# Performance work log

Hardware: AMD Instinct MI355X
Metric: run time of the kernel (lower is better)

## Reference

```python
import jax, jax.numpy as jnp
import numpy as np

S = 4          # num_segments
T = 4096       # frames
D = 1024       # input_size == output_size
HEADS = 1
FREQ = 10000.0
DH = D // HEADS     # per-head width = 1024
TB = T // S         # block height = 1024
WB = DH // S        # block width  = 256


def _abs_pos(tb, d, freq):
    # Matches getAbsolutePosition: AP[p, 2i] = sin(p / freq^(2i/d)), AP[p, 2i+1] = cos(same).
    pos = jnp.arange(tb, dtype=jnp.float32)[:, None]          # [tb,1]
    i = jnp.arange(tb // 2, dtype=jnp.float32)[None, :]       # [1,tb//2]
    ang = pos / jnp.power(jnp.float32(freq), 2.0 * i / d)     # [tb,tb//2]
    ap = jnp.zeros((tb, tb), jnp.float32)
    return ap.at[:, 0::2].set(jnp.sin(ang)).at[:, 1::2].set(jnp.cos(ang))


def setup_inputs() -> dict:
    key = jax.random.key(0)
    ks = jax.random.split(key, 6)
    x = jax.random.normal(ks[0], (T, D), jnp.float32)
    Wq = jax.random.normal(ks[1], (HEADS, DH, D), jnp.float32) * 0.02
    Wk = jax.random.normal(ks[2], (HEADS, DH, D), jnp.float32) * 0.02
    Wv = jax.random.normal(ks[3], (HEADS, DH, D), jnp.float32) * 0.02
    Wout = jax.random.normal(ks[4], (D, D), jnp.float32) * 0.02
    Wout2 = jax.random.normal(ks[5], (WB, WB + 2), jnp.float32) * 0.05
    return {"x": x, "Wq": Wq, "Wk": Wk, "Wv": Wv, "Wout": Wout, "Wout2": Wout2}


def _forward(x, Wq, Wk, Wv, Wout, Wout2):
    # diversity = 1 - cosine similarity (F.normalize p=2 along dim=1)
    xu = x / jnp.maximum(jnp.linalg.norm(x, axis=1, keepdims=True), 1e-12)
    div = 1.0 - xu @ xu.T                                     # [T,T]

    Q = jnp.einsum('ti,hdi->htd', x, Wq)                      # [h,T,DH]
    K = jnp.einsum('ti,hdi->htd', x, Wk)
    V = jnp.einsum('ti,hdi->htd', x, Wv)

    def blk(A):  # [h,T,DH] -> [h,S*S,TB,WB], block (i,j) row-major as in local_x/local_y
        return A.reshape(-1, S, TB, S, WB).transpose(0, 1, 3, 2, 4).reshape(-1, S * S, TB, WB)

    qb, kb, vb = blk(Q), blk(K), blk(V)
    # diversity uses the diagonal row-block for every column-block j of row i
    drow = jnp.stack([div[i * TB:(i + 1) * TB, i * TB:(i + 1) * TB] for i in range(S)], 0)  # [S,TB,TB]
    db = jnp.repeat(drow, S, axis=0)[None]                    # [1,S*S,TB,TB]

    sim = jnp.einsum('hbqc,hbkc->hbqk', qb, kb) + _abs_pos(TB, D, FREQ)  # [h,S*S,TB,TB]
    attw = jax.nn.softmax(sim, axis=-1)
    # normalized row entropy, then L1-normalized (F.normalize p=1)
    ent = -(attw * jax.nn.log_softmax(sim, axis=-1)).sum(-1) / jnp.log(jnp.float32(TB))  # [h,S*S,TB]
    ent = ent / jnp.maximum(jnp.abs(ent).sum(-1, keepdims=True), 1e-12)

    dep = (db * attw).sum(-1) / db.sum(-1)                    # [h,S*S,TB]
    att_win = attw + dep[:, :, None, :] * attw                # dep_factor rows are identical
    ctx = jnp.einsum('hbqk,hbkc->hbqc', att_win, vb)          # [h,S*S,TB,WB]

    chars = jax.lax.stop_gradient(jnp.stack([ent, dep], axis=-1))  # [h,S*S,TB,2] (detach)
    y = jnp.concatenate([ctx, chars], axis=-1) @ Wout2.T      # [h,S*S,TB,WB]

    # reassemble grid of blocks back to [h,T,DH], concat heads, final projection
    y = y.reshape(-1, S, S, TB, WB).transpose(0, 1, 3, 2, 4).reshape(-1, T, DH)
    y = y.transpose(1, 0, 2).reshape(T, HEADS * DH)
    return y @ Wout.T                                         # [T,D]


def reference(x, Wq, Wk, Wv, Wout, Wout2):
    return _forward(x, Wq, Wk, Wv, Wout, Wout2)
```

## Files before the change

### kernel.cpp

```cpp
#include <hip/hip_runtime.h>
#include <hip/hip_bf16.h>

#define TT 4096
#define DD 1024
#define TBB 1024
#define WBB 256

typedef __attribute__((ext_vector_type(8))) _Float16 half8;
typedef __attribute__((ext_vector_type(4))) _Float16 half4;
typedef __attribute__((ext_vector_type(16))) float f32x16;

__device__ __forceinline__ unsigned short f2h(float v) {
  _Float16 h = (_Float16)v;
  return *reinterpret_cast<unsigned short*>(&h);
}
__device__ __forceinline__ float h2f(unsigned short u) {
  _Float16 h = *reinterpret_cast<_Float16*>(&u);
  return (float)h;
}

__device__ __forceinline__ void gl_lds16(const unsigned short* g, unsigned short* l) {
  __builtin_amdgcn_global_load_lds(
      (const __attribute__((address_space(1))) void*)(unsigned long long)(g),
      (__attribute__((address_space(3))) void*)(unsigned long long)(l),
      16, 0, 0);
}

__device__ __forceinline__ float waveSum(float v) {
#pragma unroll
  for (int o = 32; o > 0; o >>= 1) v += __shfl_down(v, o, 64);
  return v;
}
__device__ __forceinline__ float waveMax(float v) {
#pragma unroll
  for (int o = 32; o > 0; o >>= 1) v = fmaxf(v, __shfl_down(v, o, 64));
  return v;
}

template <int EPI, typename OutT>
__global__ __launch_bounds__(256) void gemm_bt(
    const unsigned short* __restrict__ A, const unsigned short* __restrict__ B,
    OutT* __restrict__ C,
    int K, int lda, int ldb, int ldc,
    int zbase, int zdiv,
    long sAi, long sAj, long sBi, long sBj, long sCi, long sCj,
    long sAz, long sBz, long sCz,
    const float* __restrict__ e0, const float* __restrict__ e1,
    const float* __restrict__ e2, const float* __restrict__ e3)
{
  __shared__ __align__(16) unsigned short lA[2][4096];
  __shared__ __align__(16) unsigned short lB[2][4096];

  const int z = blockIdx.z, gz = zbase + z;
  const int zi = gz / zdiv, zj = gz - zi * zdiv;
  const unsigned short* Ab = A + (long)zi * sAi + (long)zj * sAj + (long)z * sAz;
  const unsigned short* Bb = B + (long)zi * sBi + (long)zj * sBj + (long)z * sBz;
  const long offC = (long)zi * sCi + (long)zj * sCj + (long)z * sCz;

  const int m0 = blockIdx.y * 128, n0 = blockIdx.x * 128;
  const int tid = threadIdx.x, wave = tid >> 6, lane = tid & 63;
  const int wm = (wave >> 1) * 64, wn = (wave & 1) * 64;
  const int srow = lane >> 2;
  const int scol = (((lane & 3) ^ ((srow >> 1) & 3))) * 8;
  const int l31 = lane & 31, khi = lane >> 5;
  const int sw2 = (l31 >> 1) & 3;

  f32x16 acc[2][2] = {};

  for (int k0 = 0; k0 < K; k0 += 64) {
#pragma unroll
    for (int h = 0; h < 2; ++h)
#pragma unroll
      for (int t = 0; t < 2; ++t) {
        const int r = wave * 32 + t * 16 + srow;
        gl_lds16(Ab + (long)(m0 + r) * lda + (k0 + h * 32 + scol), &lA[h][wave * 1024 + t * 512]);
        gl_lds16(Bb + (long)(n0 + r) * ldb + (k0 + h * 32 + scol), &lB[h][wave * 1024 + t * 512]);
      }
    __syncthreads();

    half8 af[2][4], bfr[2][4];
#pragma unroll
    for (int mi = 0; mi < 2; ++mi)
#pragma unroll
      for (int ks = 0; ks < 4; ++ks)
        af[mi][ks] = *(const half8*)&lA[ks >> 1][(wm + mi * 32 + l31) * 32 + ((((ks & 1) * 2 + khi) ^ sw2) * 8)];
#pragma unroll
    for (int ni = 0; ni < 2; ++ni)
#pragma unroll
      for (int ks = 0; ks < 4; ++ks)
        bfr[ni][ks] = *(const half8*)&lB[ks >> 1][(wn + ni * 32 + l31) * 32 + ((((ks & 1) * 2 + khi) ^ sw2) * 8)];

#pragma unroll
    for (int ks = 0; ks < 4; ++ks)
#pragma unroll
      for (int mi = 0; mi < 2; ++mi)
#pragma unroll
        for (int ni = 0; ni < 2; ++ni)
          acc[mi][ni] = __builtin_amdgcn_mfma_f32_32x32x16_f16(af[mi][ks], bfr[ni][ks], acc[mi][ni], 0, 0, 0);
    __syncthreads();
  }

  OutT* Cb = C + offC;
#pragma unroll
  for (int mi = 0; mi < 2; ++mi)
#pragma unroll
    for (int ni = 0; ni < 2; ++ni)
#pragma unroll
      for (int r = 0; r < 16; ++r) {
        const int row = m0 + wm + mi * 32 + khi * 4 + (r & 3) + 8 * (r >> 2);
        const int col = n0 + wn + ni * 32 + l31;
        float v = acc[mi][ni][r];
        const long ci = (long)row * ldc + col;
        if constexpr (sizeof(OutT) == 2) {
          Cb[ci] = (OutT)f2h(v);
        } else {
          Cb[ci] = v;
        }
      }
}

template <int EPI, typename OutT>
__global__ __launch_bounds__(256) void gemm_s(
    const unsigned short* __restrict__ A, const unsigned short* __restrict__ B,
    OutT* __restrict__ C,
    int K, int lda, int ldb, int ldc,
    int zbase, int zdiv,
    long sAi, long sAj, long sBi, long sBj, long sCi, long sCj,
    long sAz, long sBz, long sCz,
    const float* __restrict__ e0, const float* __restrict__ e1,
    const float* __restrict__ e2, const float* __restrict__ e3)
{
  __shared__ __align__(16) unsigned short lA[2][2048];
  __shared__ __align__(16) unsigned short lB[2][2048];

  const int z = blockIdx.z, gz = zbase + z;
  const int zi = gz / zdiv, zj = gz - zi * zdiv;
  const unsigned short* Ab = A + (long)zi * sAi + (long)zj * sAj + (long)z * sAz;
  const unsigned short* Bb = B + (long)zi * sBi + (long)zj * sBj + (long)z * sBz;
  const long offC = (long)zi * sCi + (long)zj * sCj + (long)z * sCz;

  const int m0 = blockIdx.y * 64, n0 = blockIdx.x * 64;
  const int tid = threadIdx.x, wave = tid >> 6, lane = tid & 63;
  const int wm = (wave >> 1) * 32, wn = (wave & 1) * 32;
  const int srow = lane >> 2;
  const int grow = wave * 16 + srow;
  const int scol = (((lane & 3) ^ ((grow >> 1) & 3))) * 8;
  const int l31 = lane & 31, khi = lane >> 5;
  const int sw2 = (l31 >> 1) & 3;

  f32x16 acc = {};

  for (int k0 = 0; k0 < K; k0 += 64) {
#pragma unroll
    for (int h = 0; h < 2; ++h) {
      gl_lds16(Ab + (long)(m0 + grow) * lda + (k0 + h * 32 + scol), &lA[h][wave * 512]);
      gl_lds16(Bb + (long)(n0 + grow) * ldb + (k0 + h * 32 + scol), &lB[h][wave * 512]);
    }
    __syncthreads();

    half8 af[4], bfr[4];
#pragma unroll
    for (int ks = 0; ks < 4; ++ks) {
      af[ks] = *(const half8*)&lA[ks >> 1][(wm + l31) * 32 + ((((ks & 1) * 2 + khi) ^ sw2) * 8)];
      bfr[ks] = *(const half8*)&lB[ks >> 1][(wn + l31) * 32 + ((((ks & 1) * 2 + khi) ^ sw2) * 8)];
    }
#pragma unroll
    for (int ks = 0; ks < 4; ++ks)
      acc = __builtin_amdgcn_mfma_f32_32x32x16_f16(af[ks], bfr[ks], acc, 0, 0, 0);
    __syncthreads();
  }

  OutT* Cb = C + offC;
#pragma unroll
  for (int r = 0; r < 16; ++r) {
    const int row = m0 + wm + khi * 4 + (r & 3) + 8 * (r >> 2);
    const int col = n0 + wn + l31;
    float v = acc[r];
    if constexpr (EPI == 1) v = 1.0f - v;
    if constexpr (EPI == 3)
      v += e0[(long)gz * 1024 + row] * e2[col] + e1[(long)gz * 1024 + row] * e3[col];
    const long ci = (long)row * ldc + col;
    if constexpr (sizeof(OutT) == 2) {
      Cb[ci] = (OutT)f2h(v);
    } else {
      Cb[ci] = v;
    }
  }
}

__global__ __launch_bounds__(256) void sim_gemm(
    const unsigned short* __restrict__ A, const unsigned short* __restrict__ B,
    unsigned short* __restrict__ C,
    const unsigned short* __restrict__ APh)
{
  __shared__ __align__(16) unsigned short lA[2][4096];
  __shared__ __align__(16) unsigned short lB[2][4096];

  const int gz = blockIdx.z;
  const int zi = gz >> 2, zj = gz & 3;
  const unsigned short* Ab = A + (long)zi * (TBB * DD) + zj * WBB;
  const unsigned short* Bb = B + (long)zi * (TBB * DD) + zj * WBB;
  unsigned short* Cb = C + (long)gz * TBB * TBB;

  const int m0 = blockIdx.y * 128, n0 = blockIdx.x * 128;
  const int tid = threadIdx.x, wave = tid >> 6, lane = tid & 63;
  const int wm = (wave >> 1) * 64, wn = (wave & 1) * 64;
  const int srow = lane >> 2;
  const int scol = ((lane & 3) ^ ((srow >> 1) & 3)) * 8;
  const int l31 = lane & 31, khi = lane >> 5;
  const int sw2 = (l31 >> 1) & 3;

  f32x16 acc[2][2] = {};

  for (int k0 = 0; k0 < WBB; k0 += 64) {
#pragma unroll
    for (int h = 0; h < 2; ++h)
#pragma unroll
      for (int t = 0; t < 2; ++t) {
        const int r = wave * 32 + t * 16 + srow;
        gl_lds16(Ab + (long)(m0 + r) * DD + (k0 + h * 32 + scol), &lA[h][wave * 1024 + t * 512]);
        gl_lds16(Bb + (long)(n0 + r) * DD + (k0 + h * 32 + scol), &lB[h][wave * 1024 + t * 512]);
      }
    __syncthreads();

    half8 af[2][4], bfr[2][4];
#pragma unroll
    for (int mi = 0; mi < 2; ++mi)
#pragma unroll
      for (int ks = 0; ks < 4; ++ks)
        af[mi][ks] = *(const half8*)&lA[ks >> 1][(wm + mi * 32 + l31) * 32 + ((((ks & 1) * 2 + khi) ^ sw2) * 8)];
#pragma unroll
    for (int ni = 0; ni < 2; ++ni)
#pragma unroll
      for (int ks = 0; ks < 4; ++ks)
        bfr[ni][ks] = *(const half8*)&lB[ks >> 1][(wn + ni * 32 + l31) * 32 + ((((ks & 1) * 2 + khi) ^ sw2) * 8)];

#pragma unroll
    for (int ks = 0; ks < 4; ++ks)
#pragma unroll
      for (int mi = 0; mi < 2; ++mi)
#pragma unroll
        for (int ni = 0; ni < 2; ++ni)
          acc[mi][ni] = __builtin_amdgcn_mfma_f32_32x32x16_f16(af[mi][ks], bfr[ni][ks], acc[mi][ni], 0, 0, 0);
    __syncthreads();
  }

#pragma unroll
  for (int mi = 0; mi < 2; ++mi)
#pragma unroll
    for (int ni = 0; ni < 2; ++ni)
#pragma unroll
      for (int r = 0; r < 16; ++r) {
        const int row = m0 + wm + mi * 32 + khi * 4 + (r & 3) + 8 * (r >> 2);
        const int col = n0 + wn + ni * 32 + l31;
        Cb[(long)row * TBB + col] = f2h(acc[mi][ni][r] + h2f(APh[(long)row * 1024 + col]));
      }
}

__global__ __launch_bounds__(256) void ctx_gemm_s(
    const unsigned short* __restrict__ wpre, const float* __restrict__ dep,
    const unsigned short* __restrict__ Vt, unsigned short* __restrict__ ctx)
{
  __shared__ __align__(16) unsigned short lA[2][2048];
  __shared__ __align__(16) unsigned short lB[2][2048];
  __shared__ __align__(16) unsigned short sDepH[1024];

  const int gz = blockIdx.z, zi = gz >> 2, zj = gz & 3;
  const int m0 = blockIdx.y * 64, n0 = blockIdx.x * 64;
  const int tid = threadIdx.x, wave = tid >> 6, lane = tid & 63;
  const int wm = (wave >> 1) * 32, wn = (wave & 1) * 32;
  const int srow = lane >> 2;
  const int grow = wave * 16 + srow;
  const int scol = ((lane & 3) ^ ((grow >> 1) & 3)) * 8;
  const int l31 = lane & 31, khi = lane >> 5;
  const int sw2 = (l31 >> 1) & 3;

#pragma unroll
  for (int p = 0; p < 4; ++p)
    sDepH[tid + p * 256] = f2h(1.f + dep[(long)gz * 1024 + tid + p * 256]);
  __syncthreads();

  const unsigned short* Ab = wpre + (long)gz * TBB * TBB;
  const unsigned short* Bb = Vt + (long)(zj * 256) * TT + (long)zi * 1024;

  f32x16 acc = {};

  for (int k0 = 0; k0 < 1024; k0 += 64) {
#pragma unroll
    for (int h = 0; h < 2; ++h)
      gl_lds16(Bb + (long)(n0 + grow) * TT + (k0 + h * 32 + scol), &lB[h][wave * 512]);
#pragma unroll
    for (int h = 0; h < 2; ++h)
#pragma unroll
      for (int p = 0; p < 2; ++p) {
        const int idx = p * 1024 + tid * 4;
        const int row = idx >> 5, col = idx & 31;
        ushort4 wv = *(const ushort4*)(Ab + (long)(m0 + row) * 1024 + k0 + h * 32 + col);
        const half4 dv = *(const half4*)&sDepH[k0 + h * 32 + col];
        half4 pv = *(half4*)&wv * dv;
        const int pcol = (((col >> 3) ^ ((row >> 1) & 3)) << 3) | (col & 7);
        *(half4*)&lA[h][row * 32 + pcol] = pv;
      }
    __syncthreads();

    half8 af[4], bfr[4];
#pragma unroll
    for (int ks = 0; ks < 4; ++ks) {
      af[ks] = *(const half8*)&lA[ks >> 1][(wm + l31) * 32 + ((((ks & 1) * 2 + khi) ^ sw2) * 8)];
      bfr[ks] = *(const half8*)&lB[ks >> 1][(wn + l31) * 32 + ((((ks & 1) * 2 + khi) ^ sw2) * 8)];
    }
#pragma unroll
    for (int ks = 0; ks < 4; ++ks)
      acc = __builtin_amdgcn_mfma_f32_32x32x16_f16(af[ks], bfr[ks], acc, 0, 0, 0);
    __syncthreads();
  }

  unsigned short* Cb = ctx + (long)gz * TBB * WBB;
#pragma unroll
  for (int r = 0; r < 16; ++r) {
    const int row = m0 + wm + khi * 4 + (r & 3) + 8 * (r >> 2);
    const int col = n0 + wn + l31;
    Cb[(long)row * WBB + col] = f2h(acc[r]);
  }
}

__global__ __launch_bounds__(256) void prepx_kernel(
    const float* __restrict__ x, unsigned short* __restrict__ xh,
    unsigned short* __restrict__ xu)
{
  const int t = blockIdx.x, tid = threadIdx.x;
  const float4 v = *((const float4*)(x + (long)t * DD) + tid);
  float ss = v.x * v.x + v.y * v.y + v.z * v.z + v.w * v.w;
  ss = waveSum(ss);
  __shared__ float red[4];
  if ((tid & 63) == 0) red[tid >> 6] = ss;
  __syncthreads();
  const float tot = red[0] + red[1] + red[2] + red[3];
  const float inv = 1.f / fmaxf(sqrtf(tot), 1e-12f);
  ushort4 h, u;
  h.x = f2h(v.x); h.y = f2h(v.y); h.z = f2h(v.z); h.w = f2h(v.w);
  u.x = f2h(v.x * inv); u.y = f2h(v.y * inv); u.z = f2h(v.z * inv); u.w = f2h(v.w * inv);
  *((ushort4*)(xh + (long)t * DD) + tid) = h;
  *((ushort4*)(xu + (long)t * DD) + tid) = u;
}

__global__ __launch_bounds__(256) void castw_kernel(
    const float* __restrict__ Wq, const float* __restrict__ Wk, const float* __restrict__ Wv,
    unsigned short* __restrict__ o)
{
  const long idx4 = ((long)blockIdx.x * 256 + threadIdx.x) * 4;
  const int which = (int)(idx4 >> 20);
  const long loc = idx4 & ((1L << 20) - 1);
  const float* src = (which == 0) ? Wq : ((which == 1) ? Wk : Wv);
  const float4 v = *(const float4*)(src + loc);
  ushort4 h;
  h.x = f2h(v.x); h.y = f2h(v.y); h.z = f2h(v.z); h.w = f2h(v.w);
  *(ushort4*)(o + idx4) = h;
}

__global__ __launch_bounds__(256) void castp_kernel(const float* __restrict__ src,
                                                    unsigned short* __restrict__ dst)
{
  const long idx4 = ((long)blockIdx.x * 256 + threadIdx.x) * 4;
  const float4 v = *(const float4*)(src + idx4);
  ushort4 h;
  h.x = f2h(v.x); h.y = f2h(v.y); h.z = f2h(v.z); h.w = f2h(v.w);
  *(ushort4*)(dst + idx4) = h;
}

__global__ __launch_bounds__(256) void packw2_kernel(
    const float* __restrict__ W2, unsigned short* __restrict__ W2B,
    float* __restrict__ Ecol, float* __restrict__ Dcol)
{
  const int c = blockIdx.x, j = threadIdx.x;
  W2B[c * 256 + j] = f2h(W2[c * 258 + j]);
  if (j == 0) {
    Ecol[c] = W2[c * 258 + 256];
    Dcol[c] = W2[c * 258 + 257];
  }
}

__global__ __launch_bounds__(256) void ap_kernel(unsigned short* __restrict__ APh)
{
  const int p = blockIdx.x, tid = threadIdx.x;
#pragma unroll
  for (int t = 0; t < 4; ++t) {
    const int col = tid + t * 256;
    const int i = col >> 1;
    const float e = (2.0f * (float)i) / 1024.0f;
    const float ang = (float)p / powf(10000.0f, e);
    APh[(long)p * 1024 + col] = f2h((col & 1) ? cosf(ang) : sinf(ang));
  }
}

__global__ __launch_bounds__(256) void transpose_kernel(
    const unsigned short* __restrict__ V, unsigned short* __restrict__ Vt)
{
  __shared__ unsigned short tile[32][33];
  const int tx = threadIdx.x & 31, ty = threadIdx.x >> 5;
  const int c0 = blockIdx.x * 32;
  const int r0 = blockIdx.y * 32;
#pragma unroll
  for (int rr = ty; rr < 32; rr += 8)
    tile[rr][tx] = V[(long)(r0 + rr) * DD + c0 + tx];
  __syncthreads();
#pragma unroll
  for (int rr = ty; rr < 32; rr += 8)
    Vt[(long)(c0 + rr) * TT + r0 + tx] = tile[tx][rr];
}

__global__ __launch_bounds__(256) void stats_kernel(
    const unsigned short* __restrict__ sim, const unsigned short* __restrict__ divb,
    float* __restrict__ dep, float* __restrict__ ent,
    unsigned short* __restrict__ wpre)
{
  const int q = blockIdx.x, gz = blockIdx.y, bi = gz >> 2;
  const int tid = threadIdx.x;
  const unsigned short* srow = sim + ((long)gz * TBB + q) * TBB;
  const unsigned short* drow = divb + ((long)bi * TBB + q) * TBB;
  const ushort4 sv = ((const ushort4*)srow)[tid];
  const ushort4 dv = ((const ushort4*)drow)[tid];
  float s[4] = {h2f(sv.x), h2f(sv.y), h2f(sv.z), h2f(sv.w)};
  float d[4] = {h2f(dv.x), h2f(dv.y), h2f(dv.z), h2f(dv.w)};
  float m = fmaxf(fmaxf(s[0], s[1]), fmaxf(s[2], s[3]));
  m = waveMax(m);
  __shared__ float red[4];
  if ((tid & 63) == 0) red[tid >> 6] = m;
  __syncthreads();
  m = fmaxf(fmaxf(red[0], red[1]), fmaxf(red[2], red[3]));
  float e[4];
  float l = 0.f, ss = 0.f, dn = 0.f, ds = 0.f;
#pragma unroll
  for (int p = 0; p < 4; ++p) {
    e[p] = expf(s[p] - m);
    l += e[p]; ss += e[p] * s[p]; dn += e[p] * d[p]; ds += d[p];
  }
  l = waveSum(l); ss = waveSum(ss); dn = waveSum(dn); ds = waveSum(ds);
  __shared__ float r2[16];
  if ((tid & 63) == 0) {
    const int w = tid >> 6;
    r2[w] = l; r2[4 + w] = ss; r2[8 + w] = dn; r2[12 + w] = ds;
  }
  __syncthreads();
  const float L = r2[0] + r2[1] + r2[2] + r2[3];
  const float Li = 1.f / L;
  ushort4 wq;
  wq.x = f2h(e[0] * Li); wq.y = f2h(e[1] * Li);
  wq.z = f2h(e[2] * Li); wq.w = f2h(e[3] * Li);
  ((ushort4*)(wpre + ((long)gz * TBB + q) * TBB))[tid] = wq;
  if (tid == 0) {
    const float SS = r2[4] + r2[5] + r2[6] + r2[7];
    const float DN = r2[8] + r2[9] + r2[10] + r2[11];
    const float DS = r2[12] + r2[13] + r2[14] + r2[15];
    const long o = (long)gz * TBB + q;
    dep[o] = (DN * Li) / DS;
    ent[o] = (m + logf(L) - SS * Li) * 0.14426950408889634f;
  }
}

__global__ __launch_bounds__(256) void entnorm_kernel(float* __restrict__ ent)
{
  const int gz = blockIdx.x, tid = threadIdx.x;
  float s = 0.f;
#pragma unroll
  for (int p = 0; p < 4; ++p) s += fabsf(ent[(long)gz * TBB + tid + p * 256]);
  s = waveSum(s);
  __shared__ float red[4];
  if ((tid & 63) == 0) red[tid >> 6] = s;
  __syncthreads();
  const float scale = 1.f / fmaxf(red[0] + red[1] + red[2] + red[3], 1e-12f);
#pragma unroll
  for (int p = 0; p < 4; ++p) ent[(long)gz * TBB + tid + p * 256] *= scale;
}

extern "C" void kernel_launch(void* const* d_in, const int* in_sizes, int n_in,
                              void* d_out, int out_size, void* d_ws, size_t ws_size,
                              hipStream_t stream)
{
  const float* x  = (const float*)d_in[0];
  const float* Wq = (const float*)d_in[1];
  const float* Wk = (const float*)d_in[2];
  const float* Wv = (const float*)d_in[3];
  const float* Wo = (const float*)d_in[4];
  const float* W2 = (const float*)d_in[5];

  char* ws = (char*)d_ws;
  size_t off = 0;
  auto take = [&](size_t bytes) -> void* {
    void* p = ws + off;
    off += (bytes + 255) & ~(size_t)255;
    return p;
  };
  unsigned short* QKV = (unsigned short*)take((size_t)3 * TT * DD * 2);
  unsigned short* xh  = (unsigned short*)take((size_t)TT * DD * 2);
  unsigned short* xu  = (unsigned short*)take((size_t)TT * DD * 2);
  unsigned short* Wh  = (unsigned short*)take((size_t)3 * DD * DD * 2);
  unsigned short* WoB = (unsigned short*)take((size_t)DD * DD * 2);
  unsigned short* W2B = (unsigned short*)take((size_t)256 * 256 * 2);
  float* Ecol = (float*)take(256 * 4);
  float* Dcol = (float*)take(256 * 4);
  unsigned short* APh = (unsigned short*)take((size_t)TBB * TBB * 2);
  unsigned short* divb = (unsigned short*)take((size_t)4 * TBB * TBB * 2);
  unsigned short* Vt = (unsigned short*)take((size_t)DD * TT * 2);
  unsigned short* simh = (unsigned short*)take((size_t)16 * TBB * TBB * 2);
  unsigned short* wpre = (unsigned short*)take((size_t)16 * TBB * TBB * 2);
  float* depb = (float*)take((size_t)16 * TBB * 4);
  float* entb = (float*)take((size_t)16 * TBB * 4);
  unsigned short* ctx = (unsigned short*)take((size_t)16 * TBB * WBB * 2);
  unsigned short* Y = (unsigned short*)take((size_t)TT * DD * 2);
  (void)ws_size; (void)in_sizes; (void)n_in; (void)out_size;

  prepx_kernel<<<TT, 256, 0, stream>>>(x, xh, xu);
  castw_kernel<<<(3 * DD * DD) / 1024, 256, 0, stream>>>(Wq, Wk, Wv, Wh);
  castp_kernel<<<(DD * DD) / 1024, 256, 0, stream>>>(Wo, WoB);
  packw2_kernel<<<256, 256, 0, stream>>>(W2, W2B, Ecol, Dcol);
  ap_kernel<<<TBB, 256, 0, stream>>>(APh);

  gemm_bt<0, unsigned short><<<dim3(DD / 128, TT / 128, 3), 256, 0, stream>>>(
      xh, Wh, QKV,
      DD, DD, DD, DD, 0, 1,
      0, 0, (long)DD * DD, 0, (long)TT * DD, 0,
      0, 0, 0, nullptr, nullptr, nullptr, nullptr);

  transpose_kernel<<<dim3(DD / 32, TT / 32), 256, 0, stream>>>(QKV + (size_t)2 * TT * DD, Vt);

  gemm_s<1, unsigned short><<<dim3(16, 16, 4), 256, 0, stream>>>(
      xu, xu, divb,
      DD, DD, DD, TBB, 0, 1,
      (long)TBB * DD, 0, (long)TBB * DD, 0, (long)TBB * TBB, 0,
      0, 0, 0, nullptr, nullptr, nullptr, nullptr);

  const unsigned short* Qh = QKV;
  const unsigned short* Kh = QKV + (size_t)TT * DD;

  sim_gemm<<<dim3(8, 8, 16), 256, 0, stream>>>(Qh, Kh, simh, APh);

  stats_kernel<<<dim3(TBB, 16), 256, 0, stream>>>(simh, divb, depb, entb, wpre);
  entnorm_kernel<<<16, 256, 0, stream>>>(entb);

  ctx_gemm_s<<<dim3(4, 16, 16), 256, 0, stream>>>(wpre, depb, Vt, ctx);

  gemm_s<3, unsigned short><<<dim3(4, 16, 16), 256, 0, stream>>>(
      ctx, W2B, Y,
      WBB, WBB, WBB, DD, 0, 4,
      (long)4 * TBB * WBB, (long)TBB * WBB, 0, 0, (long)TBB * DD, (long)WBB,
      0, 0, 0, entb, depb, Ecol, Dcol);

  gemm_s<0, float><<<dim3(16, 64, 1), 256, 0, stream>>>(
      Y, WoB, (float*)d_out,
      DD, DD, DD, DD, 0, 1,
      0, 0, 0, 0, 0, 0,
      0, 0, 0, nullptr, nullptr, nullptr, nullptr);
}
```

Measured before the change: 266.3 us.

## Fuse softmax statistics into sim GEMM epilogue and recompute exp in ctx GEMM

The sim GEMM epilogue now computes exp(sim) and accumulates per-row sums of exp, exp*sim and exp*div with atomics, and the div GEMM accumulates row sums of div the same way. This replaces the row-wise stats kernel and the separate wpre buffer. The ctx GEMM recomputes the softmax weights from simh, using the 1/L factor and the dependency factor, while it loads the A tile. This removes a full pass over the 16x1024x1024 sim tensor and the write of wpre. In exchange it skips max-subtraction, which risks overflow if logits are large, and adds atomic contention. The Wo cast is also merged into castw, and a small zero kernel is added for the accumulators.

Result: slower. 295.5 us (+11.0%).

```diff
diff --git a/kernel.cpp b/kernel.cpp
--- a/kernel.cpp
+++ b/kernel.cpp
@@ -31,31 +31,20 @@
   for (int o = 32; o > 0; o >>= 1) v += __shfl_down(v, o, 64);
   return v;
 }
-__device__ __forceinline__ float waveMax(float v) {
-#pragma unroll
-  for (int o = 32; o > 0; o >>= 1) v = fmaxf(v, __shfl_down(v, o, 64));
-  return v;
-}
-
-template <int EPI, typename OutT>
+
 __global__ __launch_bounds__(256) void gemm_bt(
     const unsigned short* __restrict__ A, const unsigned short* __restrict__ B,
-    OutT* __restrict__ C,
+    unsigned short* __restrict__ C,
     int K, int lda, int ldb, int ldc,
-    int zbase, int zdiv,
-    long sAi, long sAj, long sBi, long sBj, long sCi, long sCj,
-    long sAz, long sBz, long sCz,
-    const float* __restrict__ e0, const float* __restrict__ e1,
-    const float* __restrict__ e2, const float* __restrict__ e3)
+    long sBz, long sCz)
 {
   __shared__ __align__(16) unsigned short lA[2][4096];
   __shared__ __align__(16) unsigned short lB[2][4096];
 
-  const int z = blockIdx.z, gz = zbase + z;
-  const int zi = gz / zdiv, zj = gz - zi * zdiv;
-  const unsigned short* Ab = A + (long)zi * sAi + (long)zj * sAj + (long)z * sAz;
-  const unsigned short* Bb = B + (long)zi * sBi + (long)zj * sBj + (long)z * sBz;
-  const long offC = (long)zi * sCi + (long)zj * sCj + (long)z * sCz;
+  const int z = blockIdx.z;
+  const unsigned short* Ab = A;
+  const unsigned short* Bb = B + (long)z * sBz;
+  unsigned short* Cb = C + (long)z * sCz;
 
   const int m0 = blockIdx.y * 128, n0 = blockIdx.x * 128;
   const int tid = threadIdx.x, wave = tid >> 6, lane = tid & 63;
@@ -100,7 +89,6 @@
     __syncthreads();
   }
 
-  OutT* Cb = C + offC;
 #pragma unroll
   for (int mi = 0; mi < 2; ++mi)
 #pragma unroll
@@ -109,13 +97,7 @@
       for (int r = 0; r < 16; ++r) {
         const int row = m0 + wm + mi * 32 + khi * 4 + (r & 3) + 8 * (r >> 2);
         const int col = n0 + wn + ni * 32 + l31;
-        float v = acc[mi][ni][r];
-        const long ci = (long)row * ldc + col;
-        if constexpr (sizeof(OutT) == 2) {
-          Cb[ci] = (OutT)f2h(v);
-        } else {
-          Cb[ci] = v;
-        }
+        Cb[(long)row * ldc + col] = f2h(acc[mi][ni][r]);
       }
 }
 
@@ -124,20 +106,20 @@
     const unsigned short* __restrict__ A, const unsigned short* __restrict__ B,
     OutT* __restrict__ C,
     int K, int lda, int ldb, int ldc,
-    int zbase, int zdiv,
+    int zdiv,
     long sAi, long sAj, long sBi, long sBj, long sCi, long sCj,
-    long sAz, long sBz, long sCz,
     const float* __restrict__ e0, const float* __restrict__ e1,
-    const float* __restrict__ e2, const float* __restrict__ e3)
+    const float* __restrict__ e2, const float* __restrict__ e3,
+    float* __restrict__ dsb)
 {
   __shared__ __align__(16) unsigned short lA[2][2048];
   __shared__ __align__(16) unsigned short lB[2][2048];
 
-  const int z = blockIdx.z, gz = zbase + z;
+  const int gz = blockIdx.z;
   const int zi = gz / zdiv, zj = gz - zi * zdiv;
-  const unsigned short* Ab = A + (long)zi * sAi + (long)zj * sAj + (long)z * sAz;
-  const unsigned short* Bb = B + (long)zi * sBi + (long)zj * sBj + (long)z * sBz;
-  const long offC = (long)zi * sCi + (long)zj * sCj + (long)z * sCz;
+  const unsigned short* Ab = A + (long)zi * sAi + (long)zj * sAj;
+  const unsigned short* Bb = B + (long)zi * sBi + (long)zj * sBj;
+  const long offC = (long)zi * sCi + (long)zj * sCj;
 
   const int m0 = blockIdx.y * 64, n0 = blockIdx.x * 64;
   const int tid = threadIdx.x, wave = tid >> 6, lane = tid & 63;
@@ -185,13 +167,20 @@
     } else {
       Cb[ci] = v;
     }
+    if constexpr (EPI == 1) {
+      float pv = v;
+#pragma unroll
+      for (int o = 16; o > 0; o >>= 1) pv += __shfl_down(pv, o, 32);
+      if (l31 == 0) atomicAdd(&dsb[(long)gz * 1024 + row], pv);
+    }
   }
 }
 
 __global__ __launch_bounds__(256) void sim_gemm(
     const unsigned short* __restrict__ A, const unsigned short* __restrict__ B,
-    unsigned short* __restrict__ C,
-    const unsigned short* __restrict__ APh)
+    unsigned short* __restrict__ C, const unsigned short* __restrict__ APh,
+    const unsigned short* __restrict__ divb,
+    float* __restrict__ accL, float* __restrict__ accS, float* __restrict__ accD)
 {
   __shared__ __align__(16) unsigned short lA[2][4096];
   __shared__ __align__(16) unsigned short lB[2][4096];
@@ -201,6 +190,7 @@
   const unsigned short* Ab = A + (long)zi * (TBB * DD) + zj * WBB;
   const unsigned short* Bb = B + (long)zi * (TBB * DD) + zj * WBB;
   unsigned short* Cb = C + (long)gz * TBB * TBB;
+  const unsigned short* Db = divb + (long)(gz >> 2) * TBB * TBB;
 
   const int m0 = blockIdx.y * 128, n0 = blockIdx.x * 128;
   const int tid = threadIdx.x, wave = tid >> 6, lane = tid & 63;
@@ -245,25 +235,48 @@
     __syncthreads();
   }
 
+  float* aL = accL + (long)gz * 1024;
+  float* aS = accS + (long)gz * 1024;
+  float* aD = accD + (long)gz * 1024;
 #pragma unroll
   for (int mi = 0; mi < 2; ++mi)
 #pragma unroll
-    for (int ni = 0; ni < 2; ++ni)
-#pragma unroll
-      for (int r = 0; r < 16; ++r) {
-        const int row = m0 + wm + mi * 32 + khi * 4 + (r & 3) + 8 * (r >> 2);
+    for (int r = 0; r < 16; ++r) {
+      const int row = m0 + wm + mi * 32 + khi * 4 + (r & 3) + 8 * (r >> 2);
+      float pl = 0.f, ps = 0.f, pd = 0.f;
+#pragma unroll
+      for (int ni = 0; ni < 2; ++ni) {
         const int col = n0 + wn + ni * 32 + l31;
-        Cb[(long)row * TBB + col] = f2h(acc[mi][ni][r] + h2f(APh[(long)row * 1024 + col]));
-      }
+        const float v = acc[mi][ni][r] + h2f(APh[(long)row * 1024 + col]);
+        Cb[(long)row * TBB + col] = f2h(v);
+        const float e = expf(v);
+        pl += e;
+        ps += e * v;
+        pd += e * h2f(Db[(long)row * TBB + col]);
+      }
+#pragma unroll
+      for (int o = 16; o > 0; o >>= 1) {
+        pl += __shfl_down(pl, o, 32);
+        ps += __shfl_down(ps, o, 32);
+        pd += __shfl_down(pd, o, 32);
+      }
+      if (l31 == 0) {
+        atomicAdd(&aL[row], pl);
+        atomicAdd(&aS[row], ps);
+        atomicAdd(&aD[row], pd);
+      }
+    }
 }
 
 __global__ __launch_bounds__(256) void ctx_gemm_s(
-    const unsigned short* __restrict__ wpre, const float* __restrict__ dep,
+    const unsigned short* __restrict__ simh, const float* __restrict__ LiB,
+    const float* __restrict__ dep,
     const unsigned short* __restrict__ Vt, unsigned short* __restrict__ ctx)
 {
   __shared__ __align__(16) unsigned short lA[2][2048];
   __shared__ __align__(16) unsigned short lB[2][2048];
-  __shared__ __align__(16) unsigned short sDepH[1024];
+  __shared__ float sLi[64];
+  __shared__ float sDep[1024];
 
   const int gz = blockIdx.z, zi = gz >> 2, zj = gz & 3;
   const int m0 = blockIdx.y * 64, n0 = blockIdx.x * 64;
@@ -275,12 +288,13 @@
   const int l31 = lane & 31, khi = lane >> 5;
   const int sw2 = (l31 >> 1) & 3;
 
+  if (tid < 64) sLi[tid] = LiB[(long)gz * 1024 + m0 + tid];
 #pragma unroll
   for (int p = 0; p < 4; ++p)
-    sDepH[tid + p * 256] = f2h(1.f + dep[(long)gz * 1024 + tid + p * 256]);
+    sDep[tid + p * 256] = 1.f + dep[(long)gz * 1024 + tid + p * 256];
   __syncthreads();
 
-  const unsigned short* Ab = wpre + (long)gz * TBB * TBB;
+  const unsigned short* Ab = simh + (long)gz * TBB * TBB;
   const unsigned short* Bb = Vt + (long)(zj * 256) * TT + (long)zi * 1024;
 
   f32x16 acc = {};
@@ -295,11 +309,15 @@
       for (int p = 0; p < 2; ++p) {
         const int idx = p * 1024 + tid * 4;
         const int row = idx >> 5, col = idx & 31;
-        ushort4 wv = *(const ushort4*)(Ab + (long)(m0 + row) * 1024 + k0 + h * 32 + col);
-        const half4 dv = *(const half4*)&sDepH[k0 + h * 32 + col];
-        half4 pv = *(half4*)&wv * dv;
+        const ushort4 sv = *(const ushort4*)(Ab + (long)(m0 + row) * 1024 + k0 + h * 32 + col);
+        const float li = sLi[row];
+        ushort4 pv;
+        pv.x = f2h(expf(h2f(sv.x)) * li * sDep[k0 + h * 32 + col]);
+        pv.y = f2h(expf(h2f(sv.y)) * li * sDep[k0 + h * 32 + col + 1]);
+        pv.z = f2h(expf(h2f(sv.z)) * li * sDep[k0 + h * 32 + col + 2]);
+        pv.w = f2h(expf(h2f(sv.w)) * li * sDep[k0 + h * 32 + col + 3]);
         const int pcol = (((col >> 3) ^ ((row >> 1) & 3)) << 3) | (col & 7);
-        *(half4*)&lA[h][row * 32 + pcol] = pv;
+        *(ushort4*)&lA[h][row * 32 + pcol] = pv;
       }
     __syncthreads();
 
@@ -322,6 +340,12 @@
     const int col = n0 + wn + l31;
     Cb[(long)row * WBB + col] = f2h(acc[r]);
   }
+}
+
+__global__ __launch_bounds__(256) void zero_kernel(float* __restrict__ p, int n)
+{
+  const int i = blockIdx.x * 256 + threadIdx.x;
+  if (i < n) p[i] = 0.f;
 }
 
 __global__ __launch_bounds__(256) void prepx_kernel(
@@ -346,26 +370,16 @@
 
 __global__ __launch_bounds__(256) void castw_kernel(
     const float* __restrict__ Wq, const float* __restrict__ Wk, const float* __restrict__ Wv,
-    unsigned short* __restrict__ o)
+    const float* __restrict__ Wo, unsigned short* __restrict__ o)
 {
   const long idx4 = ((long)blockIdx.x * 256 + threadIdx.x) * 4;
   const int which = (int)(idx4 >> 20);
   const long loc = idx4 & ((1L << 20) - 1);
-  const float* src = (which == 0) ? Wq : ((which == 1) ? Wk : Wv);
+  const float* src = (which == 0) ? Wq : ((which == 1) ? Wk : ((which == 2) ? Wv : Wo));
   const float4 v = *(const float4*)(src + loc);
   ushort4 h;
   h.x = f2h(v.x); h.y = f2h(v.y); h.z = f2h(v.z); h.w = f2h(v.w);
   *(ushort4*)(o + idx4) = h;
-}
-
-__global__ __launch_bounds__(256) void castp_kernel(const float* __restrict__ src,
-                                                    unsigned short* __restrict__ dst)
-{
-  const long idx4 = ((long)blockIdx.x * 256 + threadIdx.x) * 4;
-  const float4 v = *(const float4*)(src + idx4);
-  ushort4 h;
-  h.x = f2h(v.x); h.y = f2h(v.y); h.z = f2h(v.z); h.w = f2h(v.w);
-  *(ushort4*)(dst + idx4) = h;
 }
 
 __global__ __launch_bounds__(256) void packw2_kernel(
@@ -409,68 +423,33 @@
     Vt[(long)(c0 + rr) * TT + r0 + tx] = tile[tx][rr];
 }
 
-__global__ __launch_bounds__(256) void stats_kernel(
-    const unsigned short* __restrict__ sim, const unsigned short* __restrict__ divb,
-    float* __restrict__ dep, float* __restrict__ ent,
-    unsigned short* __restrict__ wpre)
-{
-  const int q = blockIdx.x, gz = blockIdx.y, bi = gz >> 2;
-  const int tid = threadIdx.x;
-  const unsigned short* srow = sim + ((long)gz * TBB + q) * TBB;
-  const unsigned short* drow = divb + ((long)bi * TBB + q) * TBB;
-  const ushort4 sv = ((const ushort4*)srow)[tid];
-  const ushort4 dv = ((const ushort4*)drow)[tid];
-  float s[4] = {h2f(sv.x), h2f(sv.y), h2f(sv.z), h2f(sv.w)};
-  float d[4] = {h2f(dv.x), h2f(dv.y), h2f(dv.z), h2f(dv.w)};
-  float m = fmaxf(fmaxf(s[0], s[1]), fmaxf(s[2], s[3]));
-  m = waveMax(m);
-  __shared__ float red[4];
-  if ((tid & 63) == 0) red[tid >> 6] = m;
-  __syncthreads();
-  m = fmaxf(fmaxf(red[0], red[1]), fmaxf(red[2], red[3]));
-  float e[4];
-  float l = 0.f, ss = 0.f, dn = 0.f, ds = 0.f;
+__global__ __launch_bounds__(256) void statfin_kernel(
+    const float* __restrict__ accL, const float* __restrict__ accS,
+    const float* __restrict__ accD, const float* __restrict__ dsb,
+    float* __restrict__ LiB, float* __restrict__ dep, float* __restrict__ ent)
+{
+  const int gz = blockIdx.x, tid = threadIdx.x;
+  float er[4];
+  float s = 0.f;
 #pragma unroll
   for (int p = 0; p < 4; ++p) {
-    e[p] = expf(s[p] - m);
-    l += e[p]; ss += e[p] * s[p]; dn += e[p] * d[p]; ds += d[p];
-  }
-  l = waveSum(l); ss = waveSum(ss); dn = waveSum(dn); ds = waveSum(ds);
-  __shared__ float r2[16];
-  if ((tid & 63) == 0) {
-    const int w = tid >> 6;
-    r2[w] = l; r2[4 + w] = ss; r2[8 + w] = dn; r2[12 + w] = ds;
-  }
-  __syncthreads();
-  const float L = r2[0] + r2[1] + r2[2] + r2[3];
-  const float Li = 1.f / L;
-  ushort4 wq;
-  wq.x = f2h(e[0] * Li); wq.y = f2h(e[1] * Li);
-  wq.z = f2h(e[2] * Li); wq.w = f2h(e[3] * Li);
-  ((ushort4*)(wpre + ((long)gz * TBB + q) * TBB))[tid] = wq;
-  if (tid == 0) {
-    const float SS = r2[4] + r2[5] + r2[6] + r2[7];
-    const float DN = r2[8] + r2[9] + r2[10] + r2[11];
-    const float DS = r2[12] + r2[13] + r2[14] + r2[15];
-    const long o = (long)gz * TBB + q;
-    dep[o] = (DN * Li) / DS;
-    ent[o] = (m + logf(L) - SS * Li) * 0.14426950408889634f;
-  }
-}
-
-__global__ __launch_bounds__(256) void entnorm_kernel(float* __restrict__ ent)
-{
-  const int gz = blockIdx.x, tid = threadIdx.x;
-  float s = 0.f;
-#pragma unroll
-  for (int p = 0; p < 4; ++p) s += fabsf(ent[(long)gz * TBB + tid + p * 256]);
+    const int r = tid + p * 256;
+    const long o = (long)gz * 1024 + r;
+    const float L = accL[o];
+    const float Li = 1.f / L;
+    dep[o] = (accD[o] * Li) / dsb[(long)(gz >> 2) * 1024 + r];
+    LiB[o] = Li;
+    er[p] = (logf(L) - accS[o] * Li) * 0.14426950408889634f;
+    s += fabsf(er[p]);
+  }
   s = waveSum(s);
   __shared__ float red[4];
   if ((tid & 63) == 0) red[tid >> 6] = s;
   __syncthreads();
   const float scale = 1.f / fmaxf(red[0] + red[1] + red[2] + red[3], 1e-12f);
 #pragma unroll
-  for (int p = 0; p < 4; ++p) ent[(long)gz * TBB + tid + p * 256] *= scale;
+  for (int p = 0; p < 4; ++p)
+    ent[(long)gz * 1024 + tid + p * 256] = er[p] * scale;
 }
 
 extern "C" void kernel_launch(void* const* d_in, const int* in_sizes, int n_in,
@@ -494,8 +473,8 @@
   unsigned short* QKV = (unsigned short*)take((size_t)3 * TT * DD * 2);
   unsigned short* xh  = (unsigned short*)take((size_t)TT * DD * 2);
   unsigned short* xu  = (unsigned short*)take((size_t)TT * DD * 2);
-  unsigned short* Wh  = (unsigned short*)take((size_t)3 * DD * DD * 2);
-  unsigned short* WoB = (unsigned short*)take((size_t)DD * DD * 2);
+  unsigned short* Wh  = (unsigned short*)take((size_t)4 * DD * DD * 2);
+  unsigned short* WoB = Wh + (size_t)3 * DD * DD;
   unsigned short* W2B = (unsigned short*)take((size_t)256 * 256 * 2);
   float* Ecol = (float*)take(256 * 4);
   float* Dcol = (float*)take(256 * 4);
@@ -503,52 +482,53 @@
   unsigned short* divb = (unsigned short*)take((size_t)4 * TBB * TBB * 2);
   unsigned short* Vt = (unsigned short*)take((size_t)DD * TT * 2);
   unsigned short* simh = (unsigned short*)take((size_t)16 * TBB * TBB * 2);
-  unsigned short* wpre = (unsigned short*)take((size_t)16 * TBB * TBB * 2);
+  float* accL = (float*)take((size_t)16 * TBB * 4);
+  float* accS = (float*)take((size_t)16 * TBB * 4);
+  float* accD = (float*)take((size_t)16 * TBB * 4);
+  float* dsb  = (float*)take((size_t)4 * TBB * 4);
+  float* LiB  = (float*)take((size_t)16 * TBB * 4);
   float* depb = (float*)take((size_t)16 * TBB * 4);
   float* entb = (float*)take((size_t)16 * TBB * 4);
   unsigned short* ctx = (unsigned short*)take((size_t)16 * TBB * WBB * 2);
   unsigned short* Y = (unsigned short*)take((size_t)TT * DD * 2);
   (void)ws_size; (void)in_sizes; (void)n_in; (void)out_size;
 
+  const int nZero = (3 * 16 + 4) * TBB;
+  zero_kernel<<<(nZero + 255) / 256, 256, 0, stream>>>(accL, nZero);
   prepx_kernel<<<TT, 256, 0, stream>>>(x, xh, xu);
-  castw_kernel<<<(3 * DD * DD) / 1024, 256, 0, stream>>>(Wq, Wk, Wv, Wh);
-  castp_kernel<<<(DD * DD) / 1024, 256, 0, stream>>>(Wo, WoB);
+  castw_kernel<<<(4 * DD * DD) / 1024, 256, 0, stream>>>(Wq, Wk, Wv, Wo, Wh);
   packw2_kernel<<<256, 256, 0, stream>>>(W2, W2B, Ecol, Dcol);
   ap_kernel<<<TBB, 256, 0, stream>>>(APh);
 
-  gemm_bt<0, unsigned short><<<dim3(DD / 128, TT / 128, 3), 256, 0, stream>>>(
-      xh, Wh, QKV,
-      DD, DD, DD, DD, 0, 1,
-      0, 0, (long)DD * DD, 0, (long)TT * DD, 0,
-      0, 0, 0, nullptr, nullptr, nullptr, nullptr);
+  gemm_bt<<<dim3(DD / 128, TT / 128, 3), 256, 0, stream>>>(
+      xh, Wh, QKV, DD, DD, DD, DD, (long)DD * DD, (long)TT * DD);
 
   transpose_kernel<<<dim3(DD / 32, TT / 32), 256, 0, stream>>>(QKV + (size_t)2 * TT * DD, Vt);
 
   gemm_s<1, unsigned short><<<dim3(16, 16, 4), 256, 0, stream>>>(
       xu, xu, divb,
-      DD, DD, DD, TBB, 0, 1,
+      DD, DD, DD, TBB, 1,
       (long)TBB * DD, 0, (long)TBB * DD, 0, (long)TBB * TBB, 0,
-      0, 0, 0, nullptr, nullptr, nullptr, nullptr);
+      nullptr, nullptr, nullptr, nullptr, dsb);
 
   const unsigned short* Qh = QKV;
   const unsigned short* Kh = QKV + (size_t)TT * DD;
 
-  sim_gemm<<<dim3(8, 8, 16), 256, 0, stream>>>(Qh, Kh, simh, APh);
-
-  stats_kernel<<<dim3(TBB, 16), 256, 0, stream>>>(simh, divb, depb, entb, wpre);
-  entnorm_kernel<<<16, 256, 0, stream>>>(entb);
-
-  ctx_gemm_s<<<dim3(4, 16, 16), 256, 0, stream>>>(wpre, depb, Vt, ctx);
+  sim_gemm<<<dim3(8, 8, 16), 256, 0, stream>>>(Qh, Kh, simh, APh, divb, accL, accS, accD);
+
+  statfin_kernel<<<16, 256, 0, stream>>>(accL, accS, accD, dsb, LiB, depb, entb);
+
+  ctx_gemm_s<<<dim3(4, 16, 16), 256, 0, stream>>>(simh, LiB, depb, Vt, ctx);
 
   gemm_s<3, unsigned short><<<dim3(4, 16, 16), 256, 0, stream>>>(
       ctx, W2B, Y,
-      WBB, WBB, WBB, DD, 0, 4,
+      WBB, WBB, WBB, DD, 4,
       (long)4 * TBB * WBB, (long)TBB * WBB, 0, 0, (long)TBB * DD, (long)WBB,
-      0, 0, 0, entb, depb, Ecol, Dcol);
+      entb, depb, Ecol, Dcol, nullptr);
 
   gemm_s<0, float><<<dim3(16, 64, 1), 256, 0, stream>>>(
       Y, WoB, (float*)d_out,
-      DD, DD, DD, DD, 0, 1,
+      DD, DD, DD, DD, 1,
       0, 0, 0, 0, 0, 0,
-      0, 0, 0, nullptr, nullptr, nullptr, nullptr);
-}
+      nullptr, nullptr, nullptr, nullptr, nullptr);
+}
```

## Fold Wout2 projection into Wout via precomputed fused weight matrix

Applied to the files above, without the earlier changes.

Precomputes a fused weight Bmat combining Wout with the per-block Wout2 (and its entropy/dependency columns) so the block projection and final projection become one GEMM with K padded to 1088. The ctx GEMM writes directly into the padded activation matrix and a small kernel fills the ent/dep columns. This removes one full GEMM launch and the intermediate Y buffer at the cost of slightly longer K, extra small prep kernels, and fp16 rounding of fused weights.

Measured after the change: 268.6 us. No clear change (+0.9%).

```diff
diff --git a/kernel.cpp b/kernel.cpp
--- a/kernel.cpp
+++ b/kernel.cpp
@@ -5,6 +5,7 @@
 #define DD 1024
 #define TBB 1024
 #define WBB 256
+#define KP 1088
 
 typedef __attribute__((ext_vector_type(8))) _Float16 half8;
 typedef __attribute__((ext_vector_type(4))) _Float16 half4;
@@ -37,25 +38,19 @@
   return v;
 }
 
-template <int EPI, typename OutT>
 __global__ __launch_bounds__(256) void gemm_bt(
     const unsigned short* __restrict__ A, const unsigned short* __restrict__ B,
-    OutT* __restrict__ C,
+    unsigned short* __restrict__ C,
     int K, int lda, int ldb, int ldc,
-    int zbase, int zdiv,
-    long sAi, long sAj, long sBi, long sBj, long sCi, long sCj,
-    long sAz, long sBz, long sCz,
-    const float* __restrict__ e0, const float* __restrict__ e1,
-    const float* __restrict__ e2, const float* __restrict__ e3)
+    long sBz, long sCz)
 {
   __shared__ __align__(16) unsigned short lA[2][4096];
   __shared__ __align__(16) unsigned short lB[2][4096];
 
-  const int z = blockIdx.z, gz = zbase + z;
-  const int zi = gz / zdiv, zj = gz - zi * zdiv;
-  const unsigned short* Ab = A + (long)zi * sAi + (long)zj * sAj + (long)z * sAz;
-  const unsigned short* Bb = B + (long)zi * sBi + (long)zj * sBj + (long)z * sBz;
-  const long offC = (long)zi * sCi + (long)zj * sCj + (long)z * sCz;
+  const int z = blockIdx.z;
+  const unsigned short* Ab = A;
+  const unsigned short* Bb = B + (long)z * sBz;
+  unsigned short* Cb = C + (long)z * sCz;
 
   const int m0 = blockIdx.y * 128, n0 = blockIdx.x * 128;
   const int tid = threadIdx.x, wave = tid >> 6, lane = tid & 63;
@@ -100,7 +95,6 @@
     __syncthreads();
   }
 
-  OutT* Cb = C + offC;
 #pragma unroll
   for (int mi = 0; mi < 2; ++mi)
 #pragma unroll
@@ -109,13 +103,7 @@
       for (int r = 0; r < 16; ++r) {
         const int row = m0 + wm + mi * 32 + khi * 4 + (r & 3) + 8 * (r >> 2);
         const int col = n0 + wn + ni * 32 + l31;
-        float v = acc[mi][ni][r];
-        const long ci = (long)row * ldc + col;
-        if constexpr (sizeof(OutT) == 2) {
-          Cb[ci] = (OutT)f2h(v);
-        } else {
-          Cb[ci] = v;
-        }
+        Cb[(long)row * ldc + col] = f2h(acc[mi][ni][r]);
       }
 }
 
@@ -124,20 +112,17 @@
     const unsigned short* __restrict__ A, const unsigned short* __restrict__ B,
     OutT* __restrict__ C,
     int K, int lda, int ldb, int ldc,
-    int zbase, int zdiv,
-    long sAi, long sAj, long sBi, long sBj, long sCi, long sCj,
-    long sAz, long sBz, long sCz,
-    const float* __restrict__ e0, const float* __restrict__ e1,
-    const float* __restrict__ e2, const float* __restrict__ e3)
+    int zdiv,
+    long sAi, long sAj, long sBi, long sBj, long sCi, long sCj)
 {
   __shared__ __align__(16) unsigned short lA[2][2048];
   __shared__ __align__(16) unsigned short lB[2][2048];
 
-  const int z = blockIdx.z, gz = zbase + z;
+  const int gz = blockIdx.z;
   const int zi = gz / zdiv, zj = gz - zi * zdiv;
-  const unsigned short* Ab = A + (long)zi * sAi + (long)zj * sAj + (long)z * sAz;
-  const unsigned short* Bb = B + (long)zi * sBi + (long)zj * sBj + (long)z * sBz;
-  const long offC = (long)zi * sCi + (long)zj * sCj + (long)z * sCz;
+  const unsigned short* Ab = A + (long)zi * sAi + (long)zj * sAj;
+  const unsigned short* Bb = B + (long)zi * sBi + (long)zj * sBj;
+  const long offC = (long)zi * sCi + (long)zj * sCj;
 
   const int m0 = blockIdx.y * 64, n0 = blockIdx.x * 64;
   const int tid = threadIdx.x, wave = tid >> 6, lane = tid & 63;
@@ -177,8 +162,6 @@
     const int col = n0 + wn + l31;
     float v = acc[r];
     if constexpr (EPI == 1) v = 1.0f - v;
-    if constexpr (EPI == 3)
-      v += e0[(long)gz * 1024 + row] * e2[col] + e1[(long)gz * 1024 + row] * e3[col];
     const long ci = (long)row * ldc + col;
     if constexpr (sizeof(OutT) == 2) {
       Cb[ci] = (OutT)f2h(v);
@@ -259,7 +242,7 @@
 
 __global__ __launch_bounds__(256) void ctx_gemm_s(
     const unsigned short* __restrict__ wpre, const float* __restrict__ dep,
-    const unsigned short* __restrict__ Vt, unsigned short* __restrict__ ctx)
+    const unsigned short* __restrict__ Vt, unsigned short* __restrict__ ctxA)
 {
   __shared__ __align__(16) unsigned short lA[2][2048];
   __shared__ __align__(16) unsigned short lB[2][2048];
@@ -315,12 +298,12 @@
     __syncthreads();
   }
 
-  unsigned short* Cb = ctx + (long)gz * TBB * WBB;
+  unsigned short* Cb = ctxA + (long)zi * 1024 * KP + zj * 256;
 #pragma unroll
   for (int r = 0; r < 16; ++r) {
     const int row = m0 + wm + khi * 4 + (r & 3) + 8 * (r >> 2);
     const int col = n0 + wn + l31;
-    Cb[(long)row * WBB + col] = f2h(acc[r]);
+    Cb[(long)row * KP + col] = f2h(acc[r]);
   }
 }
 
@@ -346,38 +329,67 @@
 
 __global__ __launch_bounds__(256) void castw_kernel(
     const float* __restrict__ Wq, const float* __restrict__ Wk, const float* __restrict__ Wv,
-    unsigned short* __restrict__ o)
+    const float* __restrict__ Wo, unsigned short* __restrict__ o)
 {
   const long idx4 = ((long)blockIdx.x * 256 + threadIdx.x) * 4;
   const int which = (int)(idx4 >> 20);
   const long loc = idx4 & ((1L << 20) - 1);
-  const float* src = (which == 0) ? Wq : ((which == 1) ? Wk : Wv);
+  const float* src = (which == 0) ? Wq : ((which == 1) ? Wk : ((which == 2) ? Wv : Wo));
   const float4 v = *(const float4*)(src + loc);
   ushort4 h;
   h.x = f2h(v.x); h.y = f2h(v.y); h.z = f2h(v.z); h.w = f2h(v.w);
   *(ushort4*)(o + idx4) = h;
 }
 
-__global__ __launch_bounds__(256) void castp_kernel(const float* __restrict__ src,
-                                                    unsigned short* __restrict__ dst)
-{
-  const long idx4 = ((long)blockIdx.x * 256 + threadIdx.x) * 4;
-  const float4 v = *(const float4*)(src + idx4);
-  ushort4 h;
-  h.x = f2h(v.x); h.y = f2h(v.y); h.z = f2h(v.z); h.w = f2h(v.w);
-  *(ushort4*)(dst + idx4) = h;
-}
-
 __global__ __launch_bounds__(256) void packw2_kernel(
-    const float* __restrict__ W2, unsigned short* __restrict__ W2B,
-    float* __restrict__ Ecol, float* __restrict__ Dcol)
-{
-  const int c = blockIdx.x, j = threadIdx.x;
-  W2B[c * 256 + j] = f2h(W2[c * 258 + j]);
-  if (j == 0) {
-    Ecol[c] = W2[c * 258 + 256];
-    Dcol[c] = W2[c * 258 + 257];
-  }
+    const float* __restrict__ W2, unsigned short* __restrict__ W2T)
+{
+  const int c = blockIdx.x, n = threadIdx.x;
+  W2T[c * 256 + n] = f2h(W2[n * 258 + c]);
+}
+
+__global__ __launch_bounds__(256) void bvec_kernel(
+    const float* __restrict__ W2, const unsigned short* __restrict__ WoB,
+    unsigned short* __restrict__ Bmat)
+{
+  const int d = blockIdx.x, tid = threadIdx.x;
+  const int wave = tid >> 6;
+  const float e = W2[tid * 258 + 256], dd = W2[tid * 258 + 257];
+  float p[8];
+#pragma unroll
+  for (int zj = 0; zj < 4; ++zj) {
+    const float w = h2f(WoB[(long)d * 1024 + zj * 256 + tid]);
+    p[zj] = w * e;
+    p[4 + zj] = w * dd;
+  }
+  __shared__ float red[4][8];
+#pragma unroll
+  for (int i = 0; i < 8; ++i) {
+    const float s = waveSum(p[i]);
+    if ((tid & 63) == 0) red[wave][i] = s;
+  }
+  __syncthreads();
+  if (tid < 8) {
+    const float s = red[0][tid] + red[1][tid] + red[2][tid] + red[3][tid];
+    Bmat[(long)d * KP + 1024 + tid] = f2h(s);
+  }
+  if (tid >= 8 && tid < 64) Bmat[(long)d * KP + 1024 + tid] = 0;
+}
+
+__global__ __launch_bounds__(256) void apad_kernel(
+    const float* __restrict__ ent, const float* __restrict__ dep,
+    unsigned short* __restrict__ ctxA)
+{
+  const int t = blockIdx.x * 256 + threadIdx.x;
+  const int zi = t >> 10, row = t & 1023;
+  unsigned short* base = ctxA + (long)t * KP + 1024;
+#pragma unroll
+  for (int zj = 0; zj < 4; ++zj) {
+    base[zj] = f2h(ent[(long)((zi << 2) + zj) * 1024 + row]);
+    base[4 + zj] = f2h(dep[(long)((zi << 2) + zj) * 1024 + row]);
+  }
+#pragma unroll
+  for (int i = 8; i < 64; ++i) base[i] = 0;
 }
 
 __global__ __launch_bounds__(256) void ap_kernel(unsigned short* __restrict__ APh)
@@ -494,11 +506,10 @@
   unsigned short* QKV = (unsigned short*)take((size_t)3 * TT * DD * 2);
   unsigned short* xh  = (unsigned short*)take((size_t)TT * DD * 2);
   unsigned short* xu  = (unsigned short*)take((size_t)TT * DD * 2);
-  unsigned short* Wh  = (unsigned short*)take((size_t)3 * DD * DD * 2);
-  unsigned short* WoB = (unsigned short*)take((size_t)DD * DD * 2);
-  unsigned short* W2B = (unsigned short*)take((size_t)256 * 256 * 2);
-  float* Ecol = (float*)take(256 * 4);
-  float* Dcol = (float*)take(256 * 4);
+  unsigned short* Wh  = (unsigned short*)take((size_t)4 * DD * DD * 2);
+  unsigned short* WoB = Wh + (size_t)3 * DD * DD;
+  unsigned short* W2T = (unsigned short*)take((size_t)256 * 256 * 2);
+  unsigned short* Bmat = (unsigned short*)take((size_t)DD * KP * 2);
   unsigned short* APh = (unsigned short*)take((size_t)TBB * TBB * 2);
   unsigned short* divb = (unsigned short*)take((size_t)4 * TBB * TBB * 2);
   unsigned short* Vt = (unsigned short*)take((size_t)DD * TT * 2);
@@ -506,29 +517,29 @@
   unsigned short* wpre = (unsigned short*)take((size_t)16 * TBB * TBB * 2);
   float* depb = (float*)take((size_t)16 * TBB * 4);
   float* entb = (float*)take((size_t)16 * TBB * 4);
-  unsigned short* ctx = (unsigned short*)take((size_t)16 * TBB * WBB * 2);
-  unsigned short* Y = (unsigned short*)take((size_t)TT * DD * 2);
+  unsigned short* ctxA = (unsigned short*)take((size_t)TT * KP * 2);
   (void)ws_size; (void)in_sizes; (void)n_in; (void)out_size;
 
   prepx_kernel<<<TT, 256, 0, stream>>>(x, xh, xu);
-  castw_kernel<<<(3 * DD * DD) / 1024, 256, 0, stream>>>(Wq, Wk, Wv, Wh);
-  castp_kernel<<<(DD * DD) / 1024, 256, 0, stream>>>(Wo, WoB);
-  packw2_kernel<<<256, 256, 0, stream>>>(W2, W2B, Ecol, Dcol);
+  castw_kernel<<<(4 * DD * DD) / 1024, 256, 0, stream>>>(Wq, Wk, Wv, Wo, Wh);
+  packw2_kernel<<<256, 256, 0, stream>>>(W2, W2T);
   ap_kernel<<<TBB, 256, 0, stream>>>(APh);
 
-  gemm_bt<0, unsigned short><<<dim3(DD / 128, TT / 128, 3), 256, 0, stream>>>(
-      xh, Wh, QKV,
-      DD, DD, DD, DD, 0, 1,
-      0, 0, (long)DD * DD, 0, (long)TT * DD, 0,
-      0, 0, 0, nullptr, nullptr, nullptr, nullptr);
+  gemm_s<0, unsigned short><<<dim3(4, 16, 4), 256, 0, stream>>>(
+      WoB, W2T, Bmat,
+      256, DD, 256, KP, 1,
+      256, 0, 0, 0, 256, 0);
+  bvec_kernel<<<DD, 256, 0, stream>>>(W2, WoB, Bmat);
+
+  gemm_bt<<<dim3(DD / 128, TT / 128, 3), 256, 0, stream>>>(
+      xh, Wh, QKV, DD, DD, DD, DD, (long)DD * DD, (long)TT * DD);
 
   transpose_kernel<<<dim3(DD / 32, TT / 32), 256, 0, stream>>>(QKV + (size_t)2 * TT * DD, Vt);
 
   gemm_s<1, unsigned short><<<dim3(16, 16, 4), 256, 0, stream>>>(
       xu, xu, divb,
-      DD, DD, DD, TBB, 0, 1,
-      (long)TBB * DD, 0, (long)TBB * DD, 0, (long)TBB * TBB, 0,
-      0, 0, 0, nullptr, nullptr, nullptr, nullptr);
+      DD, DD, DD, TBB, 1,
+      (long)TBB * DD, 0, (long)TBB * DD, 0, (long)TBB * TBB, 0);
 
   const unsigned short* Qh = QKV;
   const unsigned short* Kh = QKV + (size_t)TT * DD;
@@ -537,18 +548,12 @@
 
   stats_kernel<<<dim3(TBB, 16), 256, 0, stream>>>(simh, divb, depb, entb, wpre);
   entnorm_kernel<<<16, 256, 0, stream>>>(entb);
-
-  ctx_gemm_s<<<dim3(4, 16, 16), 256, 0, stream>>>(wpre, depb, Vt, ctx);
-
-  gemm_s<3, unsigned short><<<dim3(4, 16, 16), 256, 0, stream>>>(
-      ctx, W2B, Y,
-      WBB, WBB, WBB, DD, 0, 4,
-      (long)4 * TBB * WBB, (long)TBB * WBB, 0, 0, (long)TBB * DD, (long)WBB,
-      0, 0, 0, entb, depb, Ecol, Dcol);
+  apad_kernel<<<TT / 256, 256, 0, stream>>>(entb, depb, ctxA);
+
+  ctx_gemm_s<<<dim3(4, 16, 16), 256, 0, stream>>>(wpre, depb, Vt, ctxA);
 
   gemm_s<0, float><<<dim3(16, 64, 1), 256, 0, stream>>>(
-      Y, WoB, (float*)d_out,
-      DD, DD, DD, DD, 0, 1,
-      0, 0, 0, 0, 0, 0,
-      0, 0, 0, nullptr, nullptr, nullptr, nullptr);
-}
+      ctxA, Bmat, (float*)d_out,
+      KP, KP, KP, DD, 1,
+      0, 0, 0, 0, 0, 0);
+}
```
